# Performance work log

Hardware: AMD Instinct MI355X
Metric: run time of the kernel (lower is better)

The kernel has to match this reference:

```python
import jax, jax.numpy as jnp
import numpy as np

DT = 0.1
TAU = 1.0

def setup_inputs() -> dict:
    key = jax.random.key(0)
    ks = jax.random.split(key, 5)
    B, T, IN_C, N, R, OUT_C = 64, 1024, 16, 512, 16, 8
    return {
        "Batch_Input": jax.random.normal(ks[0], (B, T, IN_C), dtype=jnp.float32),
        "In_w": jax.random.normal(ks[1], (N, IN_C), dtype=jnp.float32),
        "V_w": jax.random.normal(ks[2], (R, N), dtype=jnp.float32) / np.float32(np.sqrt(N)),
        "U_w": jax.random.normal(ks[3], (N, R), dtype=jnp.float32) / np.float32(np.sqrt(R)),
        "Out_w": jax.random.normal(ks[4], (OUT_C, N), dtype=jnp.float32),
        "hidden_0": jnp.zeros((N,), dtype=jnp.float32),
    }

def reference(Batch_Input, In_w, V_w, U_w, Out_w, hidden_0):
    # Eval-mode forward (no noise injection), faithful to the torch math.
    B, T, _ = Batch_Input.shape
    a = DT / TAU  # leak integration coefficient
    # Input projection: [B, T, in_C] @ [in_C, N] -> [B, T, N]
    Inp = jnp.einsum('bti,ni->btn', Batch_Input, In_w)
    h0 = jnp.broadcast_to(hidden_0, (B, hidden_0.shape[0]))
    Inp_t = jnp.transpose(Inp, (1, 0, 2))  # [T, B, N] for scan

    def step(h, inp_t):
        phi = jnp.tanh(h)                       # act_func = Tanh
        low = jnp.einsum('bn,rn->br', phi, V_w)  # V: N -> r
        rec = jnp.einsum('br,nr->bn', low, U_w)  # U: r -> N
        h_new = (1.0 - a) * h + a * (rec + inp_t)
        return h_new, h_new

    _, hs = jax.lax.scan(step, h0, Inp_t)       # hs: [T, B, N]
    hidden_t = jnp.transpose(hs, (1, 0, 2))      # [B, T, N]
    out = jnp.einsum('btn,on->bto', jnp.tanh(hidden_t), Out_w)  # [B, T, out_C]
    return hidden_t, out
```

## Files before the change

kernel.cpp:

```cpp
#include <hip/hip_runtime.h>

#define BATCH 64
#define TT    1024
#define INC   16
#define NN    512
#define RNK   16
#define OUTC  8

#define A_COEF 0.1f

__device__ __forceinline__ float fast_tanh(float x) {
    float e = __expf(2.0f * x);
    return 1.0f - __fdividef(2.0f, e + 1.0f);
}

__device__ __forceinline__ void lgkm_barrier() {
    asm volatile("s_waitcnt lgkmcnt(0)\n\ts_barrier" ::: "memory");
}

#define DPP_XOR1 0xB1
#define DPP_XOR2 0x4E
#define DPP_XOR7 0x141
#define DPP_XOR8 0x128
template<int CTRL>
__device__ __forceinline__ float dpp_mov(float x) {
    return __int_as_float(
        __builtin_amdgcn_update_dpp(0, __float_as_int(x), CTRL, 0xF, 0xF, true));
}

__device__ __forceinline__ float2 pk_fma_blo(float2 a, float2 b, float2 c) {
    float2 d;
    asm("v_pk_fma_f32 %0, %1, %2, %3 op_sel_hi:[1,0,1]"
        : "=v"(d) : "v"(a), "v"(b), "v"(c));
    return d;
}
__device__ __forceinline__ float2 pk_fma_bhi(float2 a, float2 b, float2 c) {
    float2 d;
    asm("v_pk_fma_f32 %0, %1, %2, %3 op_sel:[0,1,0] op_sel_hi:[1,1,1]"
        : "=v"(d) : "v"(a), "v"(b), "v"(c));
    return d;
}

__global__ __launch_bounds__(256) void inp_kernel(
    const float* __restrict__ x,
    const float* __restrict__ In_w,
    float* __restrict__ Inp)
{
    const int wv = (blockIdx.x << 2) | (threadIdx.x >> 6);
    const int p  = threadIdx.x & 63;
    const int NW = gridDim.x << 2;

    float4 W4[8][4];
    #pragma unroll
    for (int k = 0; k < 8; ++k) {
        const float4* wr = (const float4*)&In_w[(p + 64 * k) * INC];
        W4[k][0] = wr[0]; W4[k][1] = wr[1]; W4[k][2] = wr[2]; W4[k][3] = wr[3];
    }

    const int ROWS = BATCH * TT;
    for (int r = wv; r < ROWS; r += NW) {
        const float4* xr = (const float4*)(x + (size_t)r * INC);
        float4 x0 = xr[0], x1 = xr[1], x2 = xr[2], x3 = xr[3];
        #pragma unroll
        for (int k = 0; k < 8; ++k) {
            float a = W4[k][0].x * x0.x;
            float b = W4[k][0].y * x0.y;
            float c = W4[k][0].z * x0.z;
            float d = W4[k][0].w * x0.w;
            a = fmaf(W4[k][1].x, x1.x, a);
            b = fmaf(W4[k][1].y, x1.y, b);
            c = fmaf(W4[k][1].z, x1.z, c);
            d = fmaf(W4[k][1].w, x1.w, d);
            a = fmaf(W4[k][2].x, x2.x, a);
            b = fmaf(W4[k][2].y, x2.y, b);
            c = fmaf(W4[k][2].z, x2.z, c);
            d = fmaf(W4[k][2].w, x2.w, d);
            a = fmaf(W4[k][3].x, x3.x, a);
            b = fmaf(W4[k][3].y, x3.y, b);
            c = fmaf(W4[k][3].z, x3.z, c);
            d = fmaf(W4[k][3].w, x3.w, d);
            Inp[(size_t)r * NN + p + 64 * k] = (a + b) + (c + d);
        }
    }
}

__global__ __launch_bounds__(256, 1) void scan_kernel(
    const float* __restrict__ Inp,
    const float* __restrict__ V_w,
    const float* __restrict__ U_w,
    const float* __restrict__ h0,
    float* __restrict__ hidden)
{
    const int tid = threadIdx.x;
    const int b   = blockIdx.x;
    const int n0  = tid << 1;
    const int row = tid >> 4;
    const int q4  = tid & 15;

    const int b0 = q4 & 1, b1 = (q4 >> 1) & 1, b2 = (q4 >> 2) & 1, b3 = (q4 >> 3) & 1;
    const int rho4 = ((b0 ^ b2) << 3) | ((b1 ^ b2) << 2) | (b2 << 1) | b3;

    __shared__ __align__(16) float lowp[2][16][20];

    float2 Vpk[2][8];
    #pragma unroll
    for (int q = 0; q < 8; ++q) {
        const int rlo = q ^ rho4, rhi = rlo ^ 8;
        Vpk[0][q] = make_float2(V_w[rlo * NN + n0],     V_w[rhi * NN + n0]);
        Vpk[1][q] = make_float2(V_w[rlo * NN + n0 + 1], V_w[rhi * NN + n0 + 1]);
    }
    float2 Upk[16];
    #pragma unroll
    for (int s = 0; s < 16; ++s)
        Upk[s] = make_float2(U_w[n0 * RNK + (s ^ rho4)],
                             U_w[(n0 + 1) * RNK + (s ^ rho4)]);

    float2 h = *(const float2*)&h0[n0];

    const float* iA = Inp + (size_t)b * TT * NN;
    float* hb = hidden + (size_t)b * TT * NN;

    float2 c = ((const float2*)iA)[tid];
    const float2 z2 = make_float2(0.f, 0.f);

    for (int t = 0; t < TT; ++t) {
        float2 phi = make_float2(fast_tanh(h.x), fast_tanh(h.y));

        const int tn = (t + 1 < TT) ? t + 1 : t;
        float2 nx = ((const float2*)(iA + (size_t)tn * NN))[tid];

        float2 Ppk[8];
        #pragma unroll
        for (int q = 0; q < 8; ++q) {
            Ppk[q] = pk_fma_blo(Vpk[0][q], phi, z2);
            Ppk[q] = pk_fma_bhi(Vpk[1][q], phi, Ppk[q]);
        }

        #pragma unroll
        for (int q = 0; q < 8; ++q) Ppk[q].x += dpp_mov<DPP_XOR1>(Ppk[q].y);
        #pragma unroll
        for (int s = 0; s < 4; ++s) Ppk[s].x += dpp_mov<DPP_XOR2>(Ppk[s + 4].x);
        Ppk[0].x += dpp_mov<DPP_XOR7>(Ppk[2].x);
        Ppk[1].x += dpp_mov<DPP_XOR7>(Ppk[3].x);
        Ppk[0].x += dpp_mov<DPP_XOR8>(Ppk[1].x);

        lowp[t & 1][rho4][row] = Ppk[0].x;
        lgkm_barrier();

        const float4* lp = (const float4*)&lowp[t & 1][rho4][0];
        float4 s0 = lp[0], s1 = lp[1], s2 = lp[2], s3 = lp[3];
        float e0 = (s0.x + s1.x) + (s2.x + s3.x);
        float e1 = (s0.y + s1.y) + (s2.y + s3.y);
        float e2 = (s0.z + s1.z) + (s2.z + s3.z);
        float e3 = (s0.w + s1.w) + (s2.w + s3.w);
        float L = (e0 + e1) + (e2 + e3);

        float g0 = L;
        float g1 = dpp_mov<DPP_XOR8>(g0);
        float g2 = dpp_mov<DPP_XOR7>(g0);
        float g3 = dpp_mov<DPP_XOR7>(g1);
        float g4 = dpp_mov<DPP_XOR2>(g0);
        float g5 = dpp_mov<DPP_XOR2>(g1);
        float g6 = dpp_mov<DPP_XOR2>(g2);
        float g7 = dpp_mov<DPP_XOR2>(g3);
        float2 Gp[8];
        Gp[0] = make_float2(g0, g1);
        Gp[1] = make_float2(g2, g3);
        Gp[2] = make_float2(g4, g5);
        Gp[3] = make_float2(g6, g7);
        Gp[4] = make_float2(dpp_mov<DPP_XOR1>(g0), dpp_mov<DPP_XOR1>(g1));
        Gp[5] = make_float2(dpp_mov<DPP_XOR1>(g2), dpp_mov<DPP_XOR1>(g3));
        Gp[6] = make_float2(dpp_mov<DPP_XOR1>(g4), dpp_mov<DPP_XOR1>(g5));
        Gp[7] = make_float2(dpp_mov<DPP_XOR1>(g6), dpp_mov<DPP_XOR1>(g7));

        float2 recA = c, recB = z2;
        #pragma unroll
        for (int u = 0; u < 8; u += 2) {
            recA = pk_fma_blo(Upk[2 * u],     Gp[u],     recA);
            recA = pk_fma_bhi(Upk[2 * u + 1], Gp[u],     recA);
            recB = pk_fma_blo(Upk[2 * u + 2], Gp[u + 1], recB);
            recB = pk_fma_bhi(Upk[2 * u + 3], Gp[u + 1], recB);
        }
        float2 rec = make_float2(recA.x + recB.x, recA.y + recB.y);

        h.x = fmaf(A_COEF, rec.x - h.x, h.x);
        h.y = fmaf(A_COEF, rec.y - h.y, h.y);
        ((float2*)(hb + (size_t)t * NN))[tid] = h;

        c = nx;
    }
}

__device__ __forceinline__ float half_wave_sum_(float x) {
    x += dpp_mov<0x111>(x);
    x += dpp_mov<0x112>(x);
    x += dpp_mov<0x114>(x);
    x += dpp_mov<0x118>(x);
    x += dpp_mov<0x142>(x);
    return x;
}
__device__ __forceinline__ float wave_sum_(float x) {
    x = half_wave_sum_(x);
    x += dpp_mov<0x143>(x);
    return x;
}

__global__ __launch_bounds__(256) void out_kernel(
    const float* __restrict__ hidden,
    const float* __restrict__ Out_w,
    float* __restrict__ out)
{
    const int wv = (blockIdx.x << 2) | (threadIdx.x >> 6);
    const int p  = threadIdx.x & 63;
    const int NW = gridDim.x << 2;

    float Ow[OUTC][8];
    #pragma unroll
    for (int o = 0; o < OUTC; ++o) {
        float4 w0 = *(const float4*)&Out_w[o * NN + p * 4];
        float4 w1 = *(const float4*)&Out_w[o * NN + 256 + p * 4];
        Ow[o][0] = w0.x; Ow[o][1] = w0.y; Ow[o][2] = w0.z; Ow[o][3] = w0.w;
        Ow[o][4] = w1.x; Ow[o][5] = w1.y; Ow[o][6] = w1.z; Ow[o][7] = w1.w;
    }

    const int ROWS = BATCH * TT;
    for (int r = wv; r < ROWS; r += NW) {
        const float4* hp = (const float4*)(hidden + (size_t)r * NN);
        float4 a = hp[p];
        float4 c = hp[64 + p];
        float ph[8];
        ph[0] = fast_tanh(a.x); ph[1] = fast_tanh(a.y);
        ph[2] = fast_tanh(a.z); ph[3] = fast_tanh(a.w);
        ph[4] = fast_tanh(c.x); ph[5] = fast_tanh(c.y);
        ph[6] = fast_tanh(c.z); ph[7] = fast_tanh(c.w);
        #pragma unroll
        for (int o = 0; o < OUTC; ++o) {
            float sa = Ow[o][0] * ph[0];
            float sb = Ow[o][1] * ph[1];
            sa = fmaf(Ow[o][2], ph[2], sa);
            sb = fmaf(Ow[o][3], ph[3], sb);
            sa = fmaf(Ow[o][4], ph[4], sa);
            sb = fmaf(Ow[o][5], ph[5], sb);
            sa = fmaf(Ow[o][6], ph[6], sa);
            sb = fmaf(Ow[o][7], ph[7], sb);
            float s = sa + sb;
            s = wave_sum_(s);
            if (p == 63) out[(size_t)r * OUTC + o] = s;
        }
    }
}

extern "C" void kernel_launch(void* const* d_in, const int* in_sizes, int n_in,
                              void* d_out, int out_size, void* d_ws, size_t ws_size,
                              hipStream_t stream) {
    const float* x    = (const float*)d_in[0];
    const float* In_w = (const float*)d_in[1];
    const float* V_w  = (const float*)d_in[2];
    const float* U_w  = (const float*)d_in[3];
    const float* Ow   = (const float*)d_in[4];
    const float* h0   = (const float*)d_in[5];

    float* hidden = (float*)d_out;
    float* out    = hidden + (size_t)BATCH * TT * NN;
    float* Inp    = (float*)d_ws;

    inp_kernel<<<1024, 256, 0, stream>>>(x, In_w, Inp);
    scan_kernel<<<BATCH, 256, 0, stream>>>(Inp, V_w, U_w, h0, hidden);
    out_kernel<<<1024, 256, 0, stream>>>(hidden, Ow, out);
}
```

Before: 726.6 us.

## Fuse input projection and output readout into the recurrent scan kernel

```diff
diff --git a/kernel.cpp b/kernel.cpp
--- a/kernel.cpp
+++ b/kernel.cpp
@@ -17,6 +17,8 @@
 __device__ __forceinline__ void lgkm_barrier() {
     asm volatile("s_waitcnt lgkmcnt(0)\n\ts_barrier" ::: "memory");
 }
+
+#define PIN(v) asm volatile("" : "+v"(v))
 
 #define DPP_XOR1 0xB1
 #define DPP_XOR2 0x4E
@@ -41,55 +43,15 @@
     return d;
 }
 
-__global__ __launch_bounds__(256) void inp_kernel(
+__global__ __launch_bounds__(256, 1) void fused_kernel(
     const float* __restrict__ x,
     const float* __restrict__ In_w,
-    float* __restrict__ Inp)
-{
-    const int wv = (blockIdx.x << 2) | (threadIdx.x >> 6);
-    const int p  = threadIdx.x & 63;
-    const int NW = gridDim.x << 2;
-
-    float4 W4[8][4];
-    #pragma unroll
-    for (int k = 0; k < 8; ++k) {
-        const float4* wr = (const float4*)&In_w[(p + 64 * k) * INC];
-        W4[k][0] = wr[0]; W4[k][1] = wr[1]; W4[k][2] = wr[2]; W4[k][3] = wr[3];
-    }
-
-    const int ROWS = BATCH * TT;
-    for (int r = wv; r < ROWS; r += NW) {
-        const float4* xr = (const float4*)(x + (size_t)r * INC);
-        float4 x0 = xr[0], x1 = xr[1], x2 = xr[2], x3 = xr[3];
-        #pragma unroll
-        for (int k = 0; k < 8; ++k) {
-            float a = W4[k][0].x * x0.x;
-            float b = W4[k][0].y * x0.y;
-            float c = W4[k][0].z * x0.z;
-            float d = W4[k][0].w * x0.w;
-            a = fmaf(W4[k][1].x, x1.x, a);
-            b = fmaf(W4[k][1].y, x1.y, b);
-            c = fmaf(W4[k][1].z, x1.z, c);
-            d = fmaf(W4[k][1].w, x1.w, d);
-            a = fmaf(W4[k][2].x, x2.x, a);
-            b = fmaf(W4[k][2].y, x2.y, b);
-            c = fmaf(W4[k][2].z, x2.z, c);
-            d = fmaf(W4[k][2].w, x2.w, d);
-            a = fmaf(W4[k][3].x, x3.x, a);
-            b = fmaf(W4[k][3].y, x3.y, b);
-            c = fmaf(W4[k][3].z, x3.z, c);
-            d = fmaf(W4[k][3].w, x3.w, d);
-            Inp[(size_t)r * NN + p + 64 * k] = (a + b) + (c + d);
-        }
-    }
-}
-
-__global__ __launch_bounds__(256, 1) void scan_kernel(
-    const float* __restrict__ Inp,
     const float* __restrict__ V_w,
     const float* __restrict__ U_w,
+    const float* __restrict__ Out_w,
     const float* __restrict__ h0,
-    float* __restrict__ hidden)
+    float* __restrict__ hidden,
+    float* __restrict__ out)
 {
     const int tid = threadIdx.x;
     const int b   = blockIdx.x;
@@ -99,8 +61,19 @@
 
     const int b0 = q4 & 1, b1 = (q4 >> 1) & 1, b2 = (q4 >> 2) & 1, b3 = (q4 >> 3) & 1;
     const int rho4 = ((b0 ^ b2) << 3) | ((b1 ^ b2) << 2) | (b2 << 1) | b3;
-
+    const int rho3 = ((b0 ^ b2) << 2) | ((b1 ^ b2) << 1) | b2;
+
+    __shared__ __align__(16) float xs[TT * INC];
     __shared__ __align__(16) float lowp[2][16][20];
+    __shared__ __align__(16) float outp[2][OUTC][20];
+
+    {
+        const float4* src = (const float4*)(x + (size_t)b * TT * INC);
+        float4* dst = (float4*)xs;
+        #pragma unroll
+        for (int cc = 0; cc < 16; ++cc)
+            dst[cc * 256 + tid] = src[cc * 256 + tid];
+    }
 
     float2 Vpk[2][8];
     #pragma unroll
@@ -114,26 +87,87 @@
     for (int s = 0; s < 16; ++s)
         Upk[s] = make_float2(U_w[n0 * RNK + (s ^ rho4)],
                              U_w[(n0 + 1) * RNK + (s ^ rho4)]);
+    float2 Wcol[INC];
+    #pragma unroll
+    for (int i = 0; i < INC; ++i)
+        Wcol[i] = make_float2(In_w[n0 * INC + i], In_w[(n0 + 1) * INC + i]);
+    float2 Opk[2][4];
+    #pragma unroll
+    for (int u = 0; u < 4; ++u) {
+        const int olo = u ^ rho3, ohi = olo ^ 4;
+        Opk[0][u] = make_float2(Out_w[olo * NN + n0],     Out_w[ohi * NN + n0]);
+        Opk[1][u] = make_float2(Out_w[olo * NN + n0 + 1], Out_w[ohi * NN + n0 + 1]);
+    }
+
+    #pragma unroll
+    for (int q = 0; q < 8; ++q) {
+        PIN(Vpk[0][q].x); PIN(Vpk[0][q].y); PIN(Vpk[1][q].x); PIN(Vpk[1][q].y);
+    }
+    #pragma unroll
+    for (int s = 0; s < 16; ++s) { PIN(Upk[s].x); PIN(Upk[s].y); }
+    #pragma unroll
+    for (int i = 0; i < INC; ++i) { PIN(Wcol[i].x); PIN(Wcol[i].y); }
+    #pragma unroll
+    for (int u = 0; u < 4; ++u) {
+        PIN(Opk[0][u].x); PIN(Opk[0][u].y); PIN(Opk[1][u].x); PIN(Opk[1][u].y);
+    }
 
     float2 h = *(const float2*)&h0[n0];
 
-    const float* iA = Inp + (size_t)b * TT * NN;
     float* hb = hidden + (size_t)b * TT * NN;
-
-    float2 c = ((const float2*)iA)[tid];
+    float* ob = out + (size_t)b * TT * OUTC;
+
+    __syncthreads();
+
     const float2 z2 = make_float2(0.f, 0.f);
 
     for (int t = 0; t < TT; ++t) {
+        const float4* xp = (const float4*)(xs + t * INC);
+        float4 xv0 = xp[0], xv1 = xp[1], xv2 = xp[2], xv3 = xp[3];
+
         float2 phi = make_float2(fast_tanh(h.x), fast_tanh(h.y));
-
-        const int tn = (t + 1 < TT) ? t + 1 : t;
-        float2 nx = ((const float2*)(iA + (size_t)tn * NN))[tid];
 
         float2 Ppk[8];
         #pragma unroll
         for (int q = 0; q < 8; ++q) {
             Ppk[q] = pk_fma_blo(Vpk[0][q], phi, z2);
             Ppk[q] = pk_fma_bhi(Vpk[1][q], phi, Ppk[q]);
+        }
+
+        float2 opk[4];
+        #pragma unroll
+        for (int u = 0; u < 4; ++u) {
+            opk[u] = pk_fma_blo(Opk[0][u], phi, z2);
+            opk[u] = pk_fma_bhi(Opk[1][u], phi, opk[u]);
+        }
+
+        float2 ipk;
+        {
+            float2 xp0 = make_float2(xv0.x, xv0.y);
+            float2 xp1 = make_float2(xv0.z, xv0.w);
+            float2 xp2 = make_float2(xv1.x, xv1.y);
+            float2 xp3 = make_float2(xv1.z, xv1.w);
+            float2 xp4 = make_float2(xv2.x, xv2.y);
+            float2 xp5 = make_float2(xv2.z, xv2.w);
+            float2 xp6 = make_float2(xv3.x, xv3.y);
+            float2 xp7 = make_float2(xv3.z, xv3.w);
+            float2 iA = pk_fma_blo(Wcol[0], xp0, z2);
+            iA = pk_fma_bhi(Wcol[1],  xp0, iA);
+            float2 iB = pk_fma_blo(Wcol[2], xp1, z2);
+            iB = pk_fma_bhi(Wcol[3],  xp1, iB);
+            iA = pk_fma_blo(Wcol[4],  xp2, iA);
+            iA = pk_fma_bhi(Wcol[5],  xp2, iA);
+            iB = pk_fma_blo(Wcol[6],  xp3, iB);
+            iB = pk_fma_bhi(Wcol[7],  xp3, iB);
+            iA = pk_fma_blo(Wcol[8],  xp4, iA);
+            iA = pk_fma_bhi(Wcol[9],  xp4, iA);
+            iB = pk_fma_blo(Wcol[10], xp5, iB);
+            iB = pk_fma_bhi(Wcol[11], xp5, iB);
+            iA = pk_fma_blo(Wcol[12], xp6, iA);
+            iA = pk_fma_bhi(Wcol[13], xp6, iA);
+            iB = pk_fma_blo(Wcol[14], xp7, iB);
+            iB = pk_fma_bhi(Wcol[15], xp7, iB);
+            ipk = make_float2(iA.x + iB.x, iA.y + iB.y);
         }
 
         #pragma unroll
@@ -143,8 +177,16 @@
         Ppk[0].x += dpp_mov<DPP_XOR7>(Ppk[2].x);
         Ppk[1].x += dpp_mov<DPP_XOR7>(Ppk[3].x);
         Ppk[0].x += dpp_mov<DPP_XOR8>(Ppk[1].x);
-
         lowp[t & 1][rho4][row] = Ppk[0].x;
+
+        #pragma unroll
+        for (int u = 0; u < 4; ++u) opk[u].x += dpp_mov<DPP_XOR1>(opk[u].y);
+        opk[0].x += dpp_mov<DPP_XOR2>(opk[2].x);
+        opk[1].x += dpp_mov<DPP_XOR2>(opk[3].x);
+        opk[0].x += dpp_mov<DPP_XOR7>(opk[1].x);
+        opk[0].x += dpp_mov<DPP_XOR8>(opk[0].x);
+        if (q4 < 8) outp[t & 1][rho3][row] = opk[0].x;
+
         lgkm_barrier();
 
         const float4* lp = (const float4*)&lowp[t & 1][rho4][0];
@@ -173,7 +215,7 @@
         Gp[6] = make_float2(dpp_mov<DPP_XOR1>(g4), dpp_mov<DPP_XOR1>(g5));
         Gp[7] = make_float2(dpp_mov<DPP_XOR1>(g6), dpp_mov<DPP_XOR1>(g7));
 
-        float2 recA = c, recB = z2;
+        float2 recA = ipk, recB = z2;
         #pragma unroll
         for (int u = 0; u < 8; u += 2) {
             recA = pk_fma_blo(Upk[2 * u],     Gp[u],     recA);
@@ -187,65 +229,41 @@
         h.y = fmaf(A_COEF, rec.y - h.y, h.y);
         ((float2*)(hb + (size_t)t * NN))[tid] = h;
 
-        c = nx;
-    }
-}
-
-__device__ __forceinline__ float half_wave_sum_(float x) {
-    x += dpp_mov<0x111>(x);
-    x += dpp_mov<0x112>(x);
-    x += dpp_mov<0x114>(x);
-    x += dpp_mov<0x118>(x);
-    x += dpp_mov<0x142>(x);
-    return x;
-}
-__device__ __forceinline__ float wave_sum_(float x) {
-    x = half_wave_sum_(x);
-    x += dpp_mov<0x143>(x);
-    return x;
-}
-
-__global__ __launch_bounds__(256) void out_kernel(
-    const float* __restrict__ hidden,
-    const float* __restrict__ Out_w,
-    float* __restrict__ out)
-{
-    const int wv = (blockIdx.x << 2) | (threadIdx.x >> 6);
-    const int p  = threadIdx.x & 63;
-    const int NW = gridDim.x << 2;
-
-    float Ow[OUTC][8];
-    #pragma unroll
-    for (int o = 0; o < OUTC; ++o) {
-        float4 w0 = *(const float4*)&Out_w[o * NN + p * 4];
-        float4 w1 = *(const float4*)&Out_w[o * NN + 256 + p * 4];
-        Ow[o][0] = w0.x; Ow[o][1] = w0.y; Ow[o][2] = w0.z; Ow[o][3] = w0.w;
-        Ow[o][4] = w1.x; Ow[o][5] = w1.y; Ow[o][6] = w1.z; Ow[o][7] = w1.w;
-    }
-
-    const int ROWS = BATCH * TT;
-    for (int r = wv; r < ROWS; r += NW) {
-        const float4* hp = (const float4*)(hidden + (size_t)r * NN);
-        float4 a = hp[p];
-        float4 c = hp[64 + p];
-        float ph[8];
-        ph[0] = fast_tanh(a.x); ph[1] = fast_tanh(a.y);
-        ph[2] = fast_tanh(a.z); ph[3] = fast_tanh(a.w);
-        ph[4] = fast_tanh(c.x); ph[5] = fast_tanh(c.y);
-        ph[6] = fast_tanh(c.z); ph[7] = fast_tanh(c.w);
-        #pragma unroll
-        for (int o = 0; o < OUTC; ++o) {
-            float sa = Ow[o][0] * ph[0];
-            float sb = Ow[o][1] * ph[1];
-            sa = fmaf(Ow[o][2], ph[2], sa);
-            sb = fmaf(Ow[o][3], ph[3], sb);
-            sa = fmaf(Ow[o][4], ph[4], sa);
-            sb = fmaf(Ow[o][5], ph[5], sb);
-            sa = fmaf(Ow[o][6], ph[6], sa);
-            sb = fmaf(Ow[o][7], ph[7], sb);
-            float s = sa + sb;
-            s = wave_sum_(s);
-            if (p == 63) out[(size_t)r * OUTC + o] = s;
+        if (t > 0 && tid < 8) {
+            const float4* op = (const float4*)&outp[t & 1][tid][0];
+            float4 o0 = op[0], o1 = op[1], o2 = op[2], o3 = op[3];
+            float f0 = (o0.x + o1.x) + (o2.x + o3.x);
+            float f1 = (o0.y + o1.y) + (o2.y + o3.y);
+            float f2 = (o0.z + o1.z) + (o2.z + o3.z);
+            float f3 = (o0.w + o1.w) + (o2.w + o3.w);
+            ob[(size_t)(t - 1) * OUTC + tid] = (f0 + f1) + (f2 + f3);
+        }
+    }
+
+    {
+        float2 phi = make_float2(fast_tanh(h.x), fast_tanh(h.y));
+        float2 opk[4];
+        #pragma unroll
+        for (int u = 0; u < 4; ++u) {
+            opk[u] = pk_fma_blo(Opk[0][u], phi, z2);
+            opk[u] = pk_fma_bhi(Opk[1][u], phi, opk[u]);
+        }
+        #pragma unroll
+        for (int u = 0; u < 4; ++u) opk[u].x += dpp_mov<DPP_XOR1>(opk[u].y);
+        opk[0].x += dpp_mov<DPP_XOR2>(opk[2].x);
+        opk[1].x += dpp_mov<DPP_XOR2>(opk[3].x);
+        opk[0].x += dpp_mov<DPP_XOR7>(opk[1].x);
+        opk[0].x += dpp_mov<DPP_XOR8>(opk[0].x);
+        if (q4 < 8) outp[TT & 1][rho3][row] = opk[0].x;
+        lgkm_barrier();
+        if (tid < 8) {
+            const float4* op = (const float4*)&outp[TT & 1][tid][0];
+            float4 o0 = op[0], o1 = op[1], o2 = op[2], o3 = op[3];
+            float f0 = (o0.x + o1.x) + (o2.x + o3.x);
+            float f1 = (o0.y + o1.y) + (o2.y + o3.y);
+            float f2 = (o0.z + o1.z) + (o2.z + o3.z);
+            float f3 = (o0.w + o1.w) + (o2.w + o3.w);
+            ob[(size_t)(TT - 1) * OUTC + tid] = (f0 + f1) + (f2 + f3);
         }
     }
 }
@@ -262,9 +280,7 @@
 
     float* hidden = (float*)d_out;
     float* out    = hidden + (size_t)BATCH * TT * NN;
-    float* Inp    = (float*)d_ws;
-
-    inp_kernel<<<1024, 256, 0, stream>>>(x, In_w, Inp);
-    scan_kernel<<<BATCH, 256, 0, stream>>>(Inp, V_w, U_w, h0, hidden);
-    out_kernel<<<1024, 256, 0, stream>>>(hidden, Ow, out);
-}
+
+    fused_kernel<<<BATCH, 256, 0, stream>>>(x, In_w, V_w, U_w, Ow, h0,
+                                            hidden, out);
+}
```

After: 747.3 us. 2.8% more time.
